# Kernel tuning notes

Measured on AMD Instinct MI355X. Metric: run time of the kernel, lower is better.

Reference implementation:

```python
import jax, jax.numpy as jnp
import numpy as np

B, S, E, H, LD, P, NC = 4, 256, 256, 8, 128, 256, 2
N = S * P  # total points (static)
EPS = 1e-5


def setup_inputs() -> dict:
    key = jax.random.key(0)
    ks = jax.random.split(key, 12)
    r = lambda i, shape, s: jax.random.normal(ks[i], shape, jnp.float32) * s
    return dict(
        gl_feats=jax.random.normal(ks[0], (S, B, E), jnp.float32),
        lo_feats=jax.random.normal(ks[1], (B, N, LD), jnp.float32),
        centroids=jax.random.normal(ks[2], (B, S, 2), jnp.float32),
        np_cluster=jnp.full((S,), P, jnp.int32),
        fc1_w=r(3, (16, 2), 0.5), fc1_b=jnp.zeros(16, jnp.float32),
        fc2_w=r(4, (E, 16), 0.1), fc2_b=jnp.zeros(E, jnp.float32),
        in_proj_w=r(5, (3 * E, E), 0.05), in_proj_b=jnp.zeros(3 * E, jnp.float32),
        out_proj_w=r(6, (E, E), 0.05), out_proj_b=jnp.zeros(E, jnp.float32),
        conv2_w=r(7, (E // 2, LD + E), 0.05), conv2_b=jnp.zeros(E // 2, jnp.float32),
        bn2_gamma=jnp.ones(E // 2, jnp.float32), bn2_beta=jnp.zeros(E // 2, jnp.float32),
        bn2_mean=jnp.zeros(E // 2, jnp.float32), bn2_var=jnp.ones(E // 2, jnp.float32),
        conv3_w=r(8, (64, E // 2), 0.05), conv3_b=jnp.zeros(64, jnp.float32),
        bn3_gamma=jnp.ones(64, jnp.float32), bn3_beta=jnp.zeros(64, jnp.float32),
        bn3_mean=jnp.zeros(64, jnp.float32), bn3_var=jnp.ones(64, jnp.float32),
        conv4_w=r(9, (NC, 64), 0.05), conv4_b=jnp.zeros(NC, jnp.float32),
    )


def _bn(z, g, b, m, v):
    # inference-mode BatchNorm1d over the channel (last) axis
    return (z - m) * jax.lax.rsqrt(v + EPS) * g + b


def reference(gl_feats, lo_feats, centroids, np_cluster,
              fc1_w, fc1_b, fc2_w, fc2_b,
              in_proj_w, in_proj_b, out_proj_w, out_proj_b,
              conv2_w, conv2_b, bn2_gamma, bn2_beta, bn2_mean, bn2_var,
              conv3_w, conv3_b, bn3_gamma, bn3_beta, bn3_mean, bn3_var,
              conv4_w, conv4_b):
    # positional encoding of centroids: Linear(2,16) -> leaky_relu -> Linear(16,E)
    h = centroids @ fc1_w.T + fc1_b                      # [B,S,16]
    h = jnp.where(h >= 0, h, 0.01 * h)                   # leaky_relu_, slope 0.01
    pos = h @ fc2_w.T + fc2_b                            # [B,S,E]
    x = gl_feats.transpose(1, 0, 2) + pos                # [B,S,E] (torch MHA is seq-first)

    # MultiheadAttention (self-attn, eval-mode dropout=identity)
    qkv = x @ in_proj_w.T + in_proj_b                    # [B,S,3E]
    q, k, v = jnp.split(qkv, 3, axis=-1)
    dh = E // H
    qh = q.reshape(B, S, H, dh)
    kh = k.reshape(B, S, H, dh)
    vh = v.reshape(B, S, H, dh)
    scores = jnp.einsum('bqhd,bkhd->bhqk', qh, kh) * (1.0 / np.sqrt(dh))
    attn = jax.nn.softmax(scores, axis=-1)               # [B,H,S,S]
    ctx = jnp.einsum('bhqk,bkhd->bqhd', attn, vh).reshape(B, S, E)
    attn_out = ctx @ out_proj_w.T + out_proj_b           # [B,S,E]

    # segment-broadcast: replace the python repeat/cat loop with a gather
    cluster_ids = jnp.repeat(jnp.arange(S), np_cluster, total_repeat_length=N)  # [N]
    global_feat = attn_out[:, cluster_ids, :]            # [B,N,E]

    pc = jnp.concatenate([lo_feats, global_feat], axis=2)  # [B,N,LD+E]
    # 1x1 Conv1d == pointwise Linear over channels
    h2 = jax.nn.relu(_bn(pc @ conv2_w.T + conv2_b, bn2_gamma, bn2_beta, bn2_mean, bn2_var))
    h3 = jax.nn.relu(_bn(h2 @ conv3_w.T + conv3_b, bn3_gamma, bn3_beta, bn3_mean, bn3_var))
    out = h3 @ conv4_w.T + conv4_b                       # [B,N,NC]
    return out.transpose(0, 2, 1)                        # [B,NC,N] to match torch layout
```

## Files before the change

### kernel.cpp

```cpp
#include <hip/hip_runtime.h>

#define B_   4
#define S_   256
#define E_   256
#define H_   8
#define LD_  128
#define N_   65536
#define NC_  2

typedef __attribute__((ext_vector_type(8))) short s8v;
typedef __attribute__((ext_vector_type(4))) float f32x4;

__device__ __forceinline__ short f2bf(float f) {
  union { float f; unsigned u; } v; v.f = f;
  unsigned r = (v.u + 0x7FFFu + ((v.u >> 16) & 1u)) >> 16;
  return (short)r;
}
__device__ __forceinline__ float bf2f(short s) {
  union { float f; unsigned u; } v; v.u = ((unsigned)(unsigned short)s) << 16;
  return v.f;
}
__device__ __forceinline__ s8v pack8(float4 a, float4 b) {
  union { s8v s; unsigned u[4]; } r;
  asm("v_cvt_pk_bf16_f32 %0, %1, %2" : "=v"(r.u[0]) : "v"(a.x), "v"(a.y));
  asm("v_cvt_pk_bf16_f32 %0, %1, %2" : "=v"(r.u[1]) : "v"(a.z), "v"(a.w));
  asm("v_cvt_pk_bf16_f32 %0, %1, %2" : "=v"(r.u[2]) : "v"(b.x), "v"(b.y));
  asm("v_cvt_pk_bf16_f32 %0, %1, %2" : "=v"(r.u[3]) : "v"(b.z), "v"(b.w));
  return r.s;
}

__global__ __launch_bounds__(256) void prep_k(
    const int* __restrict__ npc, int* __restrict__ ids,
    const float* __restrict__ ipw, const float* __restrict__ opw,
    const float* __restrict__ w2, const float* __restrict__ w3,
    const float* __restrict__ b2, const float* __restrict__ g2,
    const float* __restrict__ be2, const float* __restrict__ mu2,
    const float* __restrict__ va2,
    const float* __restrict__ b3, const float* __restrict__ g3,
    const float* __restrict__ be3, const float* __restrict__ mu3,
    const float* __restrict__ va3,
    short* __restrict__ iph, short* __restrict__ ipl,
    short* __restrict__ oph, short* __restrict__ opl,
    short* __restrict__ w2bf, short* __restrict__ w3bf,
    float* __restrict__ sc2, float* __restrict__ sh2,
    float* __restrict__ sc3, float* __restrict__ sh3,
    const float* __restrict__ gl, const float* __restrict__ cen,
    const float* __restrict__ fc1w, const float* __restrict__ fc1b,
    const float* __restrict__ fc2w, const float* __restrict__ fc2b,
    short* __restrict__ Xhi, short* __restrict__ Xlo) {
  __shared__ int red[256];
  __shared__ float hsh[16];
  int bid = blockIdx.x, t = threadIdx.x;
  if (bid < 768) {
    int i = bid * 256 + t;
    if (i < 196608) {
      float v = ipw[i]; short h = f2bf(v);
      iph[i] = h; ipl[i] = f2bf(v - bf2f(h));
    }
    if (i < 65536) {
      float v = opw[i]; short h = f2bf(v);
      oph[i] = h; opl[i] = f2bf(v - bf2f(h));
    }
    if (i < 49152) w2bf[i] = f2bf(w2[i]);
    if (i < 8192)  w3bf[i] = f2bf(w3[i]);
    if (i < 128) {
      float sc = g2[i] * rsqrtf(va2[i] + 1e-5f);
      sc2[i] = sc; sh2[i] = (b2[i] - mu2[i]) * sc + be2[i];
    }
    if (i < 64) {
      float sc = g3[i] * rsqrtf(va3[i] + 1e-5f);
      sc3[i] = sc; sh3[i] = (b3[i] - mu3[i]) * sc + be3[i];
    }
  } else if (bid <= 1024) {
    int s = bid - 768;
    int val = (s == 256) ? npc[t] : ((t < s) ? npc[t] : 0);
    red[t] = val;
    __syncthreads();
    for (int off = 128; off > 0; off >>= 1) {
      if (t < off) red[t] += red[t + off];
      __syncthreads();
    }
    int st = red[0];
    if (s < 256) {
      int en = st + npc[s]; if (en > N_) en = N_;
      for (int n = st + t; n < en; n += 256) ids[n] = s;
    } else {
      for (int n = st + t; n < N_; n += 256) ids[n] = 255;
    }
  } else {
    int bs = bid - 1025;
    int b = bs >> 8, s = bs & 255;
    if (t < 16) {
      float c0 = cen[bs * 2 + 0], c1 = cen[bs * 2 + 1];
      float v = c0 * fc1w[2 * t] + c1 * fc1w[2 * t + 1] + fc1b[t];
      hsh[t] = (v >= 0.f) ? v : 0.01f * v;
    }
    __syncthreads();
    float p = fc2b[t];
#pragma unroll
    for (int j = 0; j < 16; j++) p += hsh[j] * fc2w[t * 16 + j];
    float v = gl[((size_t)s * B_ + b) * E_ + t] + p;
    short h = f2bf(v);
    Xhi[(size_t)bs * E_ + t] = h;
    Xlo[(size_t)bs * E_ + t] = f2bf(v - bf2f(h));
  }
}

__global__ __launch_bounds__(256) void gemm_x3_k(
    const short* __restrict__ Ah, const short* __restrict__ Al,
    const short* __restrict__ Wh, const short* __restrict__ Wl,
    const float* __restrict__ bias, float* __restrict__ Cf,
    int M, int N, int K) {
  __shared__ __align__(16) short gs[18432];
  const int AH = 0, AL = 4608, WH = 9216, WL = 13824;
  int t = threadIdx.x;
  int row0 = blockIdx.x * 64, col0 = blockIdx.y * 64;
  int w = t >> 6, l = t & 63, quad = l >> 4, lr = l & 15;
  int m0 = w * 16;
  int ar = t >> 2, aq = (t & 3) * 16;
  f32x4 acc[4];
#pragma unroll
  for (int i = 0; i < 4; i++) acc[i] = (f32x4)(0.f);

  for (int kc = 0; kc < K; kc += 64) {
    __syncthreads();
    {
      size_t ra = (size_t)(row0 + ar) * K + kc + aq;
      size_t rw = (size_t)(col0 + ar) * K + kc + aq;
      *(s8v*)&gs[AH + ar * 72 + aq]     = *(const s8v*)&Ah[ra];
      *(s8v*)&gs[AH + ar * 72 + aq + 8] = *(const s8v*)&Ah[ra + 8];
      *(s8v*)&gs[AL + ar * 72 + aq]     = *(const s8v*)&Al[ra];
      *(s8v*)&gs[AL + ar * 72 + aq + 8] = *(const s8v*)&Al[ra + 8];
      *(s8v*)&gs[WH + ar * 72 + aq]     = *(const s8v*)&Wh[rw];
      *(s8v*)&gs[WH + ar * 72 + aq + 8] = *(const s8v*)&Wh[rw + 8];
      *(s8v*)&gs[WL + ar * 72 + aq]     = *(const s8v*)&Wl[rw];
      *(s8v*)&gs[WL + ar * 72 + aq + 8] = *(const s8v*)&Wl[rw + 8];
    }
    __syncthreads();
#pragma unroll
    for (int ks = 0; ks < 2; ks++) {
      int ko = ks * 32 + quad * 8;
      s8v ah = *(const s8v*)&gs[AH + (m0 + lr) * 72 + ko];
      s8v al = *(const s8v*)&gs[AL + (m0 + lr) * 72 + ko];
#pragma unroll
      for (int ct = 0; ct < 4; ct++) {
        s8v bh = *(const s8v*)&gs[WH + (ct * 16 + lr) * 72 + ko];
        s8v bl = *(const s8v*)&gs[WL + (ct * 16 + lr) * 72 + ko];
        acc[ct] = __builtin_amdgcn_mfma_f32_16x16x32_bf16(ah, bh, acc[ct], 0, 0, 0);
        acc[ct] = __builtin_amdgcn_mfma_f32_16x16x32_bf16(al, bh, acc[ct], 0, 0, 0);
        acc[ct] = __builtin_amdgcn_mfma_f32_16x16x32_bf16(ah, bl, acc[ct], 0, 0, 0);
      }
    }
  }
#pragma unroll
  for (int ct = 0; ct < 4; ct++) {
    int c = col0 + ct * 16 + lr;
    float bb = bias[c];
#pragma unroll
    for (int rg = 0; rg < 4; rg++) {
      int r = row0 + m0 + quad * 4 + rg;
      Cf[(size_t)r * N + c] = acc[ct][rg] + bb;
    }
  }
}

__global__ __launch_bounds__(256) void opgemm_k(
    const short* __restrict__ Ah, const short* __restrict__ Al,
    const short* __restrict__ Wh, const short* __restrict__ Wl,
    const float* __restrict__ bias, short* __restrict__ Cb,
    int M, int N, int K) {
  __shared__ __align__(16) short gs[18432];
  const int AH = 0, AL = 4608, WH = 9216, WL = 13824;
  int t = threadIdx.x;
  int row0 = blockIdx.x * 64, col0 = blockIdx.y * 64;
  int w = t >> 6, l = t & 63, quad = l >> 4, lr = l & 15;
  int m0 = w * 16;
  int ar = t >> 2, aq = (t & 3) * 16;
  f32x4 acc[4];
#pragma unroll
  for (int i = 0; i < 4; i++) acc[i] = (f32x4)(0.f);

  for (int kc = 0; kc < K; kc += 64) {
    __syncthreads();
    {
      size_t ra = (size_t)(row0 + ar) * K + kc + aq;
      size_t rw = (size_t)(col0 + ar) * K + kc + aq;
      *(s8v*)&gs[AH + ar * 72 + aq]     = *(const s8v*)&Ah[ra];
      *(s8v*)&gs[AH + ar * 72 + aq + 8] = *(const s8v*)&Ah[ra + 8];
      *(s8v*)&gs[AL + ar * 72 + aq]     = *(const s8v*)&Al[ra];
      *(s8v*)&gs[AL + ar * 72 + aq + 8] = *(const s8v*)&Al[ra + 8];
      *(s8v*)&gs[WH + ar * 72 + aq]     = *(const s8v*)&Wh[rw];
      *(s8v*)&gs[WH + ar * 72 + aq + 8] = *(const s8v*)&Wh[rw + 8];
      *(s8v*)&gs[WL + ar * 72 + aq]     = *(const s8v*)&Wl[rw];
      *(s8v*)&gs[WL + ar * 72 + aq + 8] = *(const s8v*)&Wl[rw + 8];
    }
    __syncthreads();
#pragma unroll
    for (int ks = 0; ks < 2; ks++) {
      int ko = ks * 32 + quad * 8;
      s8v ah = *(const s8v*)&gs[AH + (m0 + lr) * 72 + ko];
      s8v al = *(const s8v*)&gs[AL + (m0 + lr) * 72 + ko];
#pragma unroll
      for (int ct = 0; ct < 4; ct++) {
        s8v bh = *(const s8v*)&gs[WH + (ct * 16 + lr) * 72 + ko];
        s8v bl = *(const s8v*)&gs[WL + (ct * 16 + lr) * 72 + ko];
        acc[ct] = __builtin_amdgcn_mfma_f32_16x16x32_bf16(ah, bh, acc[ct], 0, 0, 0);
        acc[ct] = __builtin_amdgcn_mfma_f32_16x16x32_bf16(al, bh, acc[ct], 0, 0, 0);
        acc[ct] = __builtin_amdgcn_mfma_f32_16x16x32_bf16(ah, bl, acc[ct], 0, 0, 0);
      }
    }
  }
#pragma unroll
  for (int ct = 0; ct < 4; ct++) {
    int c = col0 + ct * 16 + lr;
    float bb = bias[c];
#pragma unroll
    for (int rg = 0; rg < 4; rg++) {
      int r = row0 + m0 + quad * 4 + rg;
      Cb[(size_t)r * N + c] = f2bf(acc[ct][rg] + bb);
    }
  }
}

__global__ __launch_bounds__(256) void gbf_k(
    const short* __restrict__ A, const short* __restrict__ w2bf,
    float* __restrict__ C) {
  __shared__ __align__(16) short gs[9216];
  const int AH = 0, BH = 4608;
  int t = threadIdx.x;
  int row0 = blockIdx.x * 64, col0 = blockIdx.y * 64;
  int w = t >> 6, l = t & 63, quad = l >> 4, lr = l & 15;
  int m0 = w * 16;
  int ar = t >> 2, aq = (t & 3) * 16;
  f32x4 acc[4];
#pragma unroll
  for (int i = 0; i < 4; i++) acc[i] = (f32x4)(0.f);

  for (int kc = 0; kc < 256; kc += 64) {
    __syncthreads();
    {
      size_t ra = (size_t)(row0 + ar) * 256 + kc + aq;
      size_t rb = (size_t)(col0 + ar) * 384 + 128 + kc + aq;
      *(s8v*)&gs[AH + ar * 72 + aq]     = *(const s8v*)&A[ra];
      *(s8v*)&gs[AH + ar * 72 + aq + 8] = *(const s8v*)&A[ra + 8];
      *(s8v*)&gs[BH + ar * 72 + aq]     = *(const s8v*)&w2bf[rb];
      *(s8v*)&gs[BH + ar * 72 + aq + 8] = *(const s8v*)&w2bf[rb + 8];
    }
    __syncthreads();
#pragma unroll
    for (int ks = 0; ks < 2; ks++) {
      int ko = ks * 32 + quad * 8;
      s8v a = *(const s8v*)&gs[AH + (m0 + lr) * 72 + ko];
#pragma unroll
      for (int ct = 0; ct < 4; ct++) {
        s8v b = *(const s8v*)&gs[BH + (ct * 16 + lr) * 72 + ko];
        acc[ct] = __builtin_amdgcn_mfma_f32_16x16x32_bf16(a, b, acc[ct], 0, 0, 0);
      }
    }
  }
#pragma unroll
  for (int ct = 0; ct < 4; ct++) {
    int c = col0 + ct * 16 + lr;
#pragma unroll
    for (int rg = 0; rg < 4; rg++) {
      int r = row0 + m0 + quad * 4 + rg;
      C[(size_t)r * 128 + c] = acc[ct][rg];
    }
  }
}

__global__ __launch_bounds__(256) void attn_k(const float* __restrict__ qkv,
                                              short* __restrict__ Chi,
                                              short* __restrict__ Clo) {
  int bid = blockIdx.x;
  int qt = bid & 7, h = (bid >> 3) & 7, b = bid >> 6;
  __shared__ __align__(16) float smem[16384];
  float* Kx = smem;
  float* Vx = smem + 8192;
  int t = threadIdx.x;
#pragma unroll
  for (int i = 0; i < 8; i++) {
    int row = i * 32 + (t >> 3);
    int d4 = (t & 7) * 4;
    const float* base = qkv + (size_t)(b * S_ + row) * 768 + h * 32 + d4;
    *(float4*)&Kx[row * 32 + d4] = *(const float4*)(base + 256);
    *(float4*)&Vx[row * 32 + d4] = *(const float4*)(base + 512);
  }
  int r = t & 31, g = t >> 5;
  float q[32];
  {
    const float* qb = qkv + (size_t)(b * S_ + qt * 32 + r) * 768 + h * 32;
#pragma unroll
    for (int d4 = 0; d4 < 32; d4 += 4) {
      float4 v = *(const float4*)(qb + d4);
      q[d4] = v.x; q[d4 + 1] = v.y; q[d4 + 2] = v.z; q[d4 + 3] = v.w;
    }
  }
  __syncthreads();
  const float scale = 0.17677669529663687f;
  int kk0 = g * 32;
  float sc[32];
  float m = -1e30f;
#pragma unroll
  for (int kk = 0; kk < 32; kk++) {
    const float* kr = &Kx[(kk0 + kk) * 32];
    float4 a = (float4){0.f, 0.f, 0.f, 0.f};
#pragma unroll
    for (int d4 = 0; d4 < 32; d4 += 4) {
      float4 kv = *(const float4*)(kr + d4);
      a.x += q[d4] * kv.x; a.y += q[d4 + 1] * kv.y;
      a.z += q[d4 + 2] * kv.z; a.w += q[d4 + 3] * kv.w;
    }
    float s = ((a.x + a.y) + (a.z + a.w)) * scale;
    sc[kk] = s;
    m = fmaxf(m, s);
  }
  float lsum = 0.f;
  float ctx[32];
#pragma unroll
  for (int d = 0; d < 32; d++) ctx[d] = 0.f;
#pragma unroll
  for (int kk = 0; kk < 32; kk++) {
    const float* vr = &Vx[(kk0 + kk) * 32];
    float p = __expf(sc[kk] - m);
    lsum += p;
#pragma unroll
    for (int d4 = 0; d4 < 32; d4 += 4) {
      float4 vv = *(const float4*)(vr + d4);
      ctx[d4] += p * vv.x; ctx[d4 + 1] += p * vv.y;
      ctx[d4 + 2] += p * vv.z; ctx[d4 + 3] += p * vv.w;
    }
  }
  __syncthreads();
  float* ctxbuf = smem;
  float* mbuf = smem + 8192;
  float* lbuf = smem + 8448;
  mbuf[g * 32 + r] = m;
  lbuf[g * 32 + r] = lsum;
#pragma unroll
  for (int d = 0; d < 32; d++)
    ctxbuf[(g * 32 + r) * 32 + ((d + r) & 31)] = ctx[d];
  __syncthreads();
  int r2 = t & 31, dq = t >> 5;
  float M = -1e30f;
#pragma unroll
  for (int gg = 0; gg < 8; gg++) M = fmaxf(M, mbuf[gg * 32 + r2]);
  float wg[8]; float L = 0.f;
#pragma unroll
  for (int gg = 0; gg < 8; gg++) {
    wg[gg] = __expf(mbuf[gg * 32 + r2] - M);
    L += lbuf[gg * 32 + r2] * wg[gg];
  }
  float invL = 1.f / L;
  size_t base = (size_t)(b * S_ + qt * 32 + r2) * E_ + h * 32;
#pragma unroll
  for (int dd = 0; dd < 4; dd++) {
    int d = dq * 4 + dd;
    float o = 0.f;
#pragma unroll
    for (int gg = 0; gg < 8; gg++)
      o += ctxbuf[(gg * 32 + r2) * 32 + ((d + r2) & 31)] * wg[gg];
    o *= invL;
    short hi = f2bf(o);
    Chi[base + d] = hi;
    Clo[base + d] = f2bf(o - bf2f(hi));
  }
}

__global__ __launch_bounds__(256, 4) void conv_fused_k(
    const float* __restrict__ lo, const float* __restrict__ G,
    const int* __restrict__ ids,
    const short* __restrict__ w2bf, const short* __restrict__ w3bf,
    const float* __restrict__ sc2, const float* __restrict__ sh2,
    const float* __restrict__ sc3, const float* __restrict__ sh3,
    const float* __restrict__ w4, const float* __restrict__ b4,
    float* __restrict__ out) {
  __shared__ __align__(16) short smem[17408];
  __shared__ int lds_ids[128];
  int t = threadIdx.x;
  int bid = blockIdx.x;
  int b = bid >> 9;
  int n0 = (bid & 511) << 7;
  int w = t >> 6, l = t & 63;
  int quad = l >> 4, lr = l & 15;
  int mh = w & 1, chh = w >> 1;
  int ar = t >> 1, akh = (t & 1) * 64;
  const float* lob = &lo[((size_t)b * N_ + n0 + ar) * LD_ + akh];

  if (t < 128) lds_ids[t] = ids[n0 + t];
  {
    float4 pf[8];
#pragma unroll
    for (int j = 0; j < 8; j++) pf[j] = *(const float4*)(lob + j * 4);
#pragma unroll
    for (int j = 0; j < 4; j++)
      *(s8v*)&smem[ar * 136 + akh + j * 8] = pack8(pf[2 * j], pf[2 * j + 1]);
#pragma unroll
    for (int j = 0; j < 8; j++) pf[j] = *(const float4*)(lob + 32 + j * 4);
#pragma unroll
    for (int j = 0; j < 4; j++)
      *(s8v*)&smem[ar * 136 + akh + 32 + j * 8] = pack8(pf[2 * j], pf[2 * j + 1]);
  }
  __syncthreads();

  f32x4 acc2[4][4];
#pragma unroll
  for (int mt = 0; mt < 4; mt++)
#pragma unroll
    for (int rg = 0; rg < 4; rg++) {
      int p = 64 * mh + 16 * mt + 4 * quad + rg;
      const float* gr = &G[((size_t)b * 256 + lds_ids[p]) * 128 + 64 * chh + lr];
#pragma unroll
      for (int ct = 0; ct < 4; ct++)
        acc2[mt][ct][rg] = gr[16 * ct];
    }

#pragma unroll
  for (int ks = 0; ks < 4; ks++) {
    int ko = ks * 32 + quad * 8;
    s8v af[4], bfr[4];
#pragma unroll
    for (int mt = 0; mt < 4; mt++)
      af[mt] = *(const s8v*)&smem[(64 * mh + 16 * mt + lr) * 136 + ko];
#pragma unroll
    for (int ct = 0; ct < 4; ct++)
      bfr[ct] = *(const s8v*)&w2bf[(size_t)(64 * chh + 16 * ct + lr) * 384 + ko];
#pragma unroll
    for (int mt = 0; mt < 4; mt++)
#pragma unroll
      for (int ct = 0; ct < 4; ct++)
        acc2[mt][ct] = __builtin_amdgcn_mfma_f32_16x16x32_bf16(af[mt], bfr[ct], acc2[mt][ct], 0, 0, 0);
  }
  __syncthreads();

#pragma unroll
  for (int ct = 0; ct < 4; ct++) {
    int c = 64 * chh + 16 * ct + lr;
    float sc = sc2[c], sh = sh2[c];
#pragma unroll
    for (int mt = 0; mt < 4; mt++)
#pragma unroll
      for (int rg = 0; rg < 4; rg++) {
        int p = 64 * mh + 16 * mt + 4 * quad + rg;
        float z = acc2[mt][ct][rg] * sc + sh;
        smem[p * 136 + c] = f2bf(fmaxf(z, 0.f));
      }
  }
  __syncthreads();

  f32x4 acc3[2][4];
#pragma unroll
  for (int i = 0; i < 2; i++)
#pragma unroll
    for (int j = 0; j < 4; j++) acc3[i][j] = (f32x4)(0.f);
#pragma unroll
  for (int ks = 0; ks < 4; ks++) {
    int ko = ks * 32 + quad * 8;
    s8v af2[2], bf3[4];
#pragma unroll
    for (int mt = 0; mt < 2; mt++)
      af2[mt] = *(const s8v*)&smem[(32 * w + 16 * mt + lr) * 136 + ko];
#pragma unroll
    for (int ct = 0; ct < 4; ct++)
      bf3[ct] = *(const s8v*)&w3bf[(size_t)(16 * ct + lr) * 128 + ko];
#pragma unroll
    for (int mt = 0; mt < 2; mt++)
#pragma unroll
      for (int ct = 0; ct < 4; ct++)
        acc3[mt][ct] = __builtin_amdgcn_mfma_f32_16x16x32_bf16(af2[mt], bf3[ct], acc3[mt][ct], 0, 0, 0);
  }
  __syncthreads();

#pragma unroll
  for (int ct = 0; ct < 4; ct++) {
    int c = 16 * ct + lr;
    float sc = sc3[c], sh = sh3[c];
#pragma unroll
    for (int mt = 0; mt < 2; mt++)
#pragma unroll
      for (int rg = 0; rg < 4; rg++) {
        int p = 32 * w + 16 * mt + 4 * quad + rg;
        float z = acc3[mt][ct][rg] * sc + sh;
        smem[p * 72 + c] = f2bf(fmaxf(z, 0.f));
      }
  }
  __syncthreads();

  {
    int c = t >> 7, p = t & 127;
    float s = b4[c];
#pragma unroll
    for (int j = 0; j < 8; j++) {
      s8v hv = *(const s8v*)&smem[p * 72 + j * 8];
#pragma unroll
      for (int e = 0; e < 8; e++)
        s += bf2f(hv[e]) * w4[c * 64 + j * 8 + e];
    }
    out[((size_t)b * NC_ + c) * N_ + n0 + p] = s;
  }
}

extern "C" void kernel_launch(void* const* d_in, const int* in_sizes, int n_in,
                              void* d_out, int out_size, void* d_ws, size_t ws_size,
                              hipStream_t stream) {
  const float* gl   = (const float*)d_in[0];
  const float* lo   = (const float*)d_in[1];
  const float* cen  = (const float*)d_in[2];
  const int*   npc  = (const int*)d_in[3];
  const float* fc1w = (const float*)d_in[4];
  const float* fc1b = (const float*)d_in[5];
  const float* fc2w = (const float*)d_in[6];
  const float* fc2b = (const float*)d_in[7];
  const float* ipw  = (const float*)d_in[8];
  const float* ipb  = (const float*)d_in[9];
  const float* opw  = (const float*)d_in[10];
  const float* opb  = (const float*)d_in[11];
  const float* w2   = (const float*)d_in[12];
  const float* b2   = (const float*)d_in[13];
  const float* g2   = (const float*)d_in[14];
  const float* be2  = (const float*)d_in[15];
  const float* mu2  = (const float*)d_in[16];
  const float* va2  = (const float*)d_in[17];
  const float* w3   = (const float*)d_in[18];
  const float* b3   = (const float*)d_in[19];
  const float* g3   = (const float*)d_in[20];
  const float* be3  = (const float*)d_in[21];
  const float* mu3  = (const float*)d_in[22];
  const float* va3  = (const float*)d_in[23];
  const float* w4   = (const float*)d_in[24];
  const float* b4   = (const float*)d_in[25];

  char* ws = (char*)d_ws;
  float* qkv  = (float*)(ws);
  short* AO   = (short*)(ws);
  short* Xhi  = (short*)(ws + 3145728);
  short* Xlo  = (short*)(ws + 3670016);
  short* Chi  = (short*)(ws + 4194304);
  short* Clo  = (short*)(ws + 4718592);
  float* G    = (float*)(ws + 5242880);
  short* iph  = (short*)(ws + 5767168);
  short* ipl  = (short*)(ws + 6160384);
  short* oph  = (short*)(ws + 6553600);
  short* opl  = (short*)(ws + 6684672);
  short* w2bf = (short*)(ws + 6815744);
  short* w3bf = (short*)(ws + 6914048);
  int*   ids  = (int*)  (ws + 6930432);
  float* sc2  = (float*)(ws + 7192576);
  float* sh2  = (float*)(ws + 7193088);
  float* sc3  = (float*)(ws + 7193600);
  float* sh3  = (float*)(ws + 7193856);
  float* out  = (float*)d_out;

  prep_k<<<2049, 256, 0, stream>>>(npc, ids, ipw, opw, w2, w3,
                                   b2, g2, be2, mu2, va2,
                                   b3, g3, be3, mu3, va3,
                                   iph, ipl, oph, opl, w2bf, w3bf,
                                   sc2, sh2, sc3, sh3,
                                   gl, cen, fc1w, fc1b, fc2w, fc2b, Xhi, Xlo);
  gemm_x3_k<<<dim3(16, 12), 256, 0, stream>>>(Xhi, Xlo, iph, ipl, ipb,
                                              qkv, B_ * S_, 768, E_);
  attn_k<<<B_ * H_ * 8, 256, 0, stream>>>(qkv, Chi, Clo);
  opgemm_k<<<dim3(16, 4), 256, 0, stream>>>(Chi, Clo, oph, opl, opb, AO,
                                            B_ * S_, 256, E_);
  gbf_k<<<dim3(16, 2), 256, 0, stream>>>(AO, w2bf, G);
  conv_fused_k<<<B_ * (N_ / 128), 256, 0, stream>>>(
      lo, G, ids, w2bf, w3bf, sc2, sh2, sc3, sh3, w4, b4, out);
}
```

Baseline: 301.2 us.

## Fold out_proj into conv2 weights and stream lo_feats directly into MFMA

```diff
diff --git a/kernel.cpp b/kernel.cpp
--- a/kernel.cpp
+++ b/kernel.cpp
@@ -12,9 +12,9 @@
 typedef __attribute__((ext_vector_type(4))) float f32x4;
 
 __device__ __forceinline__ short f2bf(float f) {
-  union { float f; unsigned u; } v; v.f = f;
-  unsigned r = (v.u + 0x7FFFu + ((v.u >> 16) & 1u)) >> 16;
-  return (short)r;
+  unsigned u;
+  asm("v_cvt_pk_bf16_f32 %0, %1, %2" : "=v"(u) : "v"(f), "v"(f));
+  return (short)u;
 }
 __device__ __forceinline__ float bf2f(short s) {
   union { float f; unsigned u; } v; v.u = ((unsigned)(unsigned short)s) << 16;
@@ -32,6 +32,7 @@
 __global__ __launch_bounds__(256) void prep_k(
     const int* __restrict__ npc, int* __restrict__ ids,
     const float* __restrict__ ipw, const float* __restrict__ opw,
+    const float* __restrict__ opb,
     const float* __restrict__ w2, const float* __restrict__ w3,
     const float* __restrict__ b2, const float* __restrict__ g2,
     const float* __restrict__ be2, const float* __restrict__ mu2,
@@ -40,7 +41,8 @@
     const float* __restrict__ be3, const float* __restrict__ mu3,
     const float* __restrict__ va3,
     short* __restrict__ iph, short* __restrict__ ipl,
-    short* __restrict__ oph, short* __restrict__ opl,
+    short* __restrict__ Mh, short* __restrict__ Ml,
+    float* __restrict__ g0v,
     short* __restrict__ w2bf, short* __restrict__ w3bf,
     float* __restrict__ sc2, float* __restrict__ sh2,
     float* __restrict__ sc3, float* __restrict__ sh3,
@@ -50,6 +52,8 @@
     short* __restrict__ Xhi, short* __restrict__ Xlo) {
   __shared__ int red[256];
   __shared__ float hsh[16];
+  __shared__ float wrow[256];
+  __shared__ float gred[256];
   int bid = blockIdx.x, t = threadIdx.x;
   if (bid < 768) {
     int i = bid * 256 + t;
@@ -57,10 +61,6 @@
       float v = ipw[i]; short h = f2bf(v);
       iph[i] = h; ipl[i] = f2bf(v - bf2f(h));
     }
-    if (i < 65536) {
-      float v = opw[i]; short h = f2bf(v);
-      oph[i] = h; opl[i] = f2bf(v - bf2f(h));
-    }
     if (i < 49152) w2bf[i] = f2bf(w2[i]);
     if (i < 8192)  w3bf[i] = f2bf(w3[i]);
     if (i < 128) {
@@ -87,7 +87,7 @@
     } else {
       for (int n = st + t; n < N_; n += 256) ids[n] = 255;
     }
-  } else {
+  } else if (bid <= 2048) {
     int bs = bid - 1025;
     int b = bs >> 8, s = bs & 255;
     if (t < 16) {
@@ -103,6 +103,24 @@
     short h = f2bf(v);
     Xhi[(size_t)bs * E_ + t] = h;
     Xlo[(size_t)bs * E_ + t] = f2bf(v - bf2f(h));
+  } else {
+    int c = bid - 2049;
+    wrow[t] = w2[c * 384 + 128 + t];
+    gred[t] = 0.f;
+    __syncthreads();
+    float acc = 0.f;
+#pragma unroll 8
+    for (int k = 0; k < 256; k++) acc += wrow[k] * opw[(size_t)k * 256 + t];
+    short h = f2bf(acc);
+    Mh[(size_t)c * 256 + t] = h;
+    Ml[(size_t)c * 256 + t] = f2bf(acc - bf2f(h));
+    gred[t] = wrow[t] * opb[t];
+    __syncthreads();
+    for (int off = 128; off > 0; off >>= 1) {
+      if (t < off) gred[t] += gred[t + off];
+      __syncthreads();
+    }
+    if (t == 0) g0v[c] = gred[0];
   }
 }
 
@@ -164,35 +182,33 @@
   }
 }
 
-__global__ __launch_bounds__(256) void opgemm_k(
+__global__ __launch_bounds__(256) void gk_k(
     const short* __restrict__ Ah, const short* __restrict__ Al,
     const short* __restrict__ Wh, const short* __restrict__ Wl,
-    const float* __restrict__ bias, short* __restrict__ Cb,
-    int M, int N, int K) {
-  __shared__ __align__(16) short gs[18432];
-  const int AH = 0, AL = 4608, WH = 9216, WL = 13824;
+    const float* __restrict__ g0v, float* __restrict__ G) {
+  __shared__ __align__(16) short gs[13824];
+  const int AH = 0, AL = 4608, WH = 9216, WL = 11520;
   int t = threadIdx.x;
-  int row0 = blockIdx.x * 64, col0 = blockIdx.y * 64;
+  int row0 = blockIdx.x * 64, col0 = blockIdx.y * 32;
   int w = t >> 6, l = t & 63, quad = l >> 4, lr = l & 15;
   int m0 = w * 16;
   int ar = t >> 2, aq = (t & 3) * 16;
-  f32x4 acc[4];
-#pragma unroll
-  for (int i = 0; i < 4; i++) acc[i] = (f32x4)(0.f);
-
-  for (int kc = 0; kc < K; kc += 64) {
+  int wr = t >> 3, wq = (t & 7) * 8;
+  f32x4 acc[2];
+#pragma unroll
+  for (int i = 0; i < 2; i++) acc[i] = (f32x4)(0.f);
+
+  for (int kc = 0; kc < 256; kc += 64) {
     __syncthreads();
     {
-      size_t ra = (size_t)(row0 + ar) * K + kc + aq;
-      size_t rw = (size_t)(col0 + ar) * K + kc + aq;
+      size_t ra = (size_t)(row0 + ar) * 256 + kc + aq;
+      size_t rw = (size_t)(col0 + wr) * 256 + kc + wq;
       *(s8v*)&gs[AH + ar * 72 + aq]     = *(const s8v*)&Ah[ra];
       *(s8v*)&gs[AH + ar * 72 + aq + 8] = *(const s8v*)&Ah[ra + 8];
       *(s8v*)&gs[AL + ar * 72 + aq]     = *(const s8v*)&Al[ra];
       *(s8v*)&gs[AL + ar * 72 + aq + 8] = *(const s8v*)&Al[ra + 8];
-      *(s8v*)&gs[WH + ar * 72 + aq]     = *(const s8v*)&Wh[rw];
-      *(s8v*)&gs[WH + ar * 72 + aq + 8] = *(const s8v*)&Wh[rw + 8];
-      *(s8v*)&gs[WL + ar * 72 + aq]     = *(const s8v*)&Wl[rw];
-      *(s8v*)&gs[WL + ar * 72 + aq + 8] = *(const s8v*)&Wl[rw + 8];
+      *(s8v*)&gs[WH + wr * 72 + wq]     = *(const s8v*)&Wh[rw];
+      *(s8v*)&gs[WL + wr * 72 + wq]     = *(const s8v*)&Wl[rw];
     }
     __syncthreads();
 #pragma unroll
@@ -201,7 +217,7 @@
       s8v ah = *(const s8v*)&gs[AH + (m0 + lr) * 72 + ko];
       s8v al = *(const s8v*)&gs[AL + (m0 + lr) * 72 + ko];
 #pragma unroll
-      for (int ct = 0; ct < 4; ct++) {
+      for (int ct = 0; ct < 2; ct++) {
         s8v bh = *(const s8v*)&gs[WH + (ct * 16 + lr) * 72 + ko];
         s8v bl = *(const s8v*)&gs[WL + (ct * 16 + lr) * 72 + ko];
         acc[ct] = __builtin_amdgcn_mfma_f32_16x16x32_bf16(ah, bh, acc[ct], 0, 0, 0);
@@ -211,60 +227,13 @@
     }
   }
 #pragma unroll
-  for (int ct = 0; ct < 4; ct++) {
+  for (int ct = 0; ct < 2; ct++) {
     int c = col0 + ct * 16 + lr;
-    float bb = bias[c];
+    float bb = g0v[c];
 #pragma unroll
     for (int rg = 0; rg < 4; rg++) {
       int r = row0 + m0 + quad * 4 + rg;
-      Cb[(size_t)r * N + c] = f2bf(acc[ct][rg] + bb);
-    }
-  }
-}
-
-__global__ __launch_bounds__(256) void gbf_k(
-    const short* __restrict__ A, const short* __restrict__ w2bf,
-    float* __restrict__ C) {
-  __shared__ __align__(16) short gs[9216];
-  const int AH = 0, BH = 4608;
-  int t = threadIdx.x;
-  int row0 = blockIdx.x * 64, col0 = blockIdx.y * 64;
-  int w = t >> 6, l = t & 63, quad = l >> 4, lr = l & 15;
-  int m0 = w * 16;
-  int ar = t >> 2, aq = (t & 3) * 16;
-  f32x4 acc[4];
-#pragma unroll
-  for (int i = 0; i < 4; i++) acc[i] = (f32x4)(0.f);
-
-  for (int kc = 0; kc < 256; kc += 64) {
-    __syncthreads();
-    {
-      size_t ra = (size_t)(row0 + ar) * 256 + kc + aq;
-      size_t rb = (size_t)(col0 + ar) * 384 + 128 + kc + aq;
-      *(s8v*)&gs[AH + ar * 72 + aq]     = *(const s8v*)&A[ra];
-      *(s8v*)&gs[AH + ar * 72 + aq + 8] = *(const s8v*)&A[ra + 8];
-      *(s8v*)&gs[BH + ar * 72 + aq]     = *(const s8v*)&w2bf[rb];
-      *(s8v*)&gs[BH + ar * 72 + aq + 8] = *(const s8v*)&w2bf[rb + 8];
-    }
-    __syncthreads();
-#pragma unroll
-    for (int ks = 0; ks < 2; ks++) {
-      int ko = ks * 32 + quad * 8;
-      s8v a = *(const s8v*)&gs[AH + (m0 + lr) * 72 + ko];
-#pragma unroll
-      for (int ct = 0; ct < 4; ct++) {
-        s8v b = *(const s8v*)&gs[BH + (ct * 16 + lr) * 72 + ko];
-        acc[ct] = __builtin_amdgcn_mfma_f32_16x16x32_bf16(a, b, acc[ct], 0, 0, 0);
-      }
-    }
-  }
-#pragma unroll
-  for (int ct = 0; ct < 4; ct++) {
-    int c = col0 + ct * 16 + lr;
-#pragma unroll
-    for (int rg = 0; rg < 4; rg++) {
-      int r = row0 + m0 + quad * 4 + rg;
-      C[(size_t)r * 128 + c] = acc[ct][rg];
+      G[(size_t)r * 128 + c] = acc[ct][rg] + bb;
     }
   }
 }
@@ -383,45 +352,39 @@
   int n0 = (bid & 511) << 7;
   int w = t >> 6, l = t & 63;
   int quad = l >> 4, lr = l & 15;
-  int mh = w & 1, chh = w >> 1;
-  int ar = t >> 1, akh = (t & 1) * 64;
-  const float* lob = &lo[((size_t)b * N_ + n0 + ar) * LD_ + akh];
-
-  if (t < 128) lds_ids[t] = ids[n0 + t];
+  int rh = w & 1, chh = w >> 1;
+
+  int id0 = ids[n0], id127 = ids[n0 + 127];
+  bool uni = (id0 == id127);
+  float gseed[4];
   {
-    float4 pf[8];
-#pragma unroll
-    for (int j = 0; j < 8; j++) pf[j] = *(const float4*)(lob + j * 4);
-#pragma unroll
-    for (int j = 0; j < 4; j++)
-      *(s8v*)&smem[ar * 136 + akh + j * 8] = pack8(pf[2 * j], pf[2 * j + 1]);
-#pragma unroll
-    for (int j = 0; j < 8; j++) pf[j] = *(const float4*)(lob + 32 + j * 4);
-#pragma unroll
-    for (int j = 0; j < 4; j++)
-      *(s8v*)&smem[ar * 136 + akh + 32 + j * 8] = pack8(pf[2 * j], pf[2 * j + 1]);
-  }
-  __syncthreads();
-
+    const float* gr = &G[((size_t)b * 256 + id0) * 128 + 64 * chh + lr];
+#pragma unroll
+    for (int ct = 0; ct < 4; ct++) gseed[ct] = gr[16 * ct];
+  }
+  if (!uni) {
+    if (t < 128) lds_ids[t] = ids[n0 + t];
+    __syncthreads();
+  }
+
+  const float* lob = &lo[((size_t)(b * N_ + n0)) * LD_];
   f32x4 acc2[4][4];
 #pragma unroll
-  for (int mt = 0; mt < 4; mt++)
-#pragma unroll
-    for (int rg = 0; rg < 4; rg++) {
-      int p = 64 * mh + 16 * mt + 4 * quad + rg;
-      const float* gr = &G[((size_t)b * 256 + lds_ids[p]) * 128 + 64 * chh + lr];
-#pragma unroll
-      for (int ct = 0; ct < 4; ct++)
-        acc2[mt][ct][rg] = gr[16 * ct];
-    }
-
+  for (int i = 0; i < 4; i++)
+#pragma unroll
+    for (int j = 0; j < 4; j++) acc2[i][j] = (f32x4)(0.f);
 #pragma unroll
   for (int ks = 0; ks < 4; ks++) {
     int ko = ks * 32 + quad * 8;
     s8v af[4], bfr[4];
 #pragma unroll
-    for (int mt = 0; mt < 4; mt++)
-      af[mt] = *(const s8v*)&smem[(64 * mh + 16 * mt + lr) * 136 + ko];
+    for (int mt = 0; mt < 4; mt++) {
+      int p = 64 * rh + 16 * mt + lr;
+      const float* ap = lob + (size_t)p * LD_ + ko;
+      float4 x = *(const float4*)ap;
+      float4 y = *(const float4*)(ap + 4);
+      af[mt] = pack8(x, y);
+    }
 #pragma unroll
     for (int ct = 0; ct < 4; ct++)
       bfr[ct] = *(const s8v*)&w2bf[(size_t)(64 * chh + 16 * ct + lr) * 384 + ko];
@@ -431,18 +394,25 @@
       for (int ct = 0; ct < 4; ct++)
         acc2[mt][ct] = __builtin_amdgcn_mfma_f32_16x16x32_bf16(af[mt], bfr[ct], acc2[mt][ct], 0, 0, 0);
   }
-  __syncthreads();
-
+
+  size_t gbase = (size_t)b * 256 * 128;
 #pragma unroll
   for (int ct = 0; ct < 4; ct++) {
     int c = 64 * chh + 16 * ct + lr;
     float sc = sc2[c], sh = sh2[c];
+    float gsh = fmaf(gseed[ct], sc, sh);
 #pragma unroll
     for (int mt = 0; mt < 4; mt++)
 #pragma unroll
       for (int rg = 0; rg < 4; rg++) {
-        int p = 64 * mh + 16 * mt + 4 * quad + rg;
-        float z = acc2[mt][ct][rg] * sc + sh;
+        int p = 64 * rh + 16 * mt + 4 * quad + rg;
+        float z;
+        if (uni) {
+          z = fmaf(acc2[mt][ct][rg], sc, gsh);
+        } else {
+          float gv = G[gbase + (size_t)lds_ids[p] * 128 + c];
+          z = fmaf(acc2[mt][ct][rg] + gv, sc, sh);
+        }
         smem[p * 136 + c] = f2bf(fmaxf(z, 0.f));
       }
   }
@@ -532,7 +502,6 @@
 
   char* ws = (char*)d_ws;
   float* qkv  = (float*)(ws);
-  short* AO   = (short*)(ws);
   short* Xhi  = (short*)(ws + 3145728);
   short* Xlo  = (short*)(ws + 3670016);
   short* Chi  = (short*)(ws + 4194304);
@@ -540,8 +509,8 @@
   float* G    = (float*)(ws + 5242880);
   short* iph  = (short*)(ws + 5767168);
   short* ipl  = (short*)(ws + 6160384);
-  short* oph  = (short*)(ws + 6553600);
-  short* opl  = (short*)(ws + 6684672);
+  short* Mh   = (short*)(ws + 6553600);
+  short* Ml   = (short*)(ws + 6684672);
   short* w2bf = (short*)(ws + 6815744);
   short* w3bf = (short*)(ws + 6914048);
   int*   ids  = (int*)  (ws + 6930432);
@@ -549,20 +518,19 @@
   float* sh2  = (float*)(ws + 7193088);
   float* sc3  = (float*)(ws + 7193600);
   float* sh3  = (float*)(ws + 7193856);
+  float* g0v  = (float*)(ws + 7194112);
   float* out  = (float*)d_out;
 
-  prep_k<<<2049, 256, 0, stream>>>(npc, ids, ipw, opw, w2, w3,
+  prep_k<<<2177, 256, 0, stream>>>(npc, ids, ipw, opw, opb, w2, w3,
                                    b2, g2, be2, mu2, va2,
                                    b3, g3, be3, mu3, va3,
-                                   iph, ipl, oph, opl, w2bf, w3bf,
+                                   iph, ipl, Mh, Ml, g0v, w2bf, w3bf,
                                    sc2, sh2, sc3, sh3,
                                    gl, cen, fc1w, fc1b, fc2w, fc2b, Xhi, Xlo);
   gemm_x3_k<<<dim3(16, 12), 256, 0, stream>>>(Xhi, Xlo, iph, ipl, ipb,
                                               qkv, B_ * S_, 768, E_);
   attn_k<<<B_ * H_ * 8, 256, 0, stream>>>(qkv, Chi, Clo);
-  opgemm_k<<<dim3(16, 4), 256, 0, stream>>>(Chi, Clo, oph, opl, opb, AO,
-                                            B_ * S_, 256, E_);
-  gbf_k<<<dim3(16, 2), 256, 0, stream>>>(AO, w2bf, G);
+  gk_k<<<dim3(16, 4), 256, 0, stream>>>(Chi, Clo, Mh, Ml, g0v, G);
   conv_fused_k<<<B_ * (N_ / 128), 256, 0, stream>>>(
       lo, G, ids, w2bf, w3bf, sc2, sh2, sc3, sh3, w4, b4, out);
 }
```

Result: slower. 328.0 us (+8.9%).
